# Optimization experiments

Hardware: AMD Instinct MI355X
Metric: run time of the kernel (lower is better)

The kernel has to match this reference:

```python
import jax, jax.numpy as jnp
import numpy as np

N = 100000   # nodes
E = 1600000  # edges
G = 1024     # graphs
V = 51       # attr_dims[0]+1 embedding rows (padding_idx=0)
EMB = 32
H = 2        # heads
D = 64       # hidden_dim (per-head out channels)
DC = H * D   # 128 = dim_conv
NEG_GAT = 0.2   # PyG GATConv default negative_slope
NEG_ACT = 0.05  # module's leaky_relu slope
LN_EPS = 1e-5


def setup_inputs() -> dict:
    key = jax.random.key(0)
    ks = jax.random.split(key, 20)
    def nrm(k, shape, scale=0.1):
        return jax.random.normal(k, shape, dtype=jnp.float32) * scale
    x = jax.random.randint(ks[0], (N, 1), 0, V)
    edge_index = jax.random.randint(ks[1], (2, E), 0, N)
    batch_idx = jnp.sort(jax.random.randint(ks[2], (N,), 0, G))
    return {
        'x': x, 'edge_index': edge_index, 'batch_idx': batch_idx,
        'emb': nrm(ks[3], (V, EMB)).at[0].set(0.0),  # padding_idx=0
        'ln_g': jnp.ones((EMB,), jnp.float32), 'ln_b': jnp.zeros((EMB,), jnp.float32),
        'W1': nrm(ks[4], (EMB, DC)), 'a_src1': nrm(ks[5], (H, D)), 'a_dst1': nrm(ks[6], (H, D)), 'b1': nrm(ks[7], (DC,)),
        'W2': nrm(ks[8], (DC, DC)), 'a_src2': nrm(ks[9], (H, D)), 'a_dst2': nrm(ks[10], (H, D)), 'b2': nrm(ks[11], (DC,)),
        'gw1': nrm(ks[12], (DC, D)), 'gb1': nrm(ks[13], (D,)),
        'gw2': nrm(ks[14], (D, 1)), 'gb2': nrm(ks[15], (1,)),
    }


def _gat_conv(xf, src, dst, W, a_src, a_dst, b):
    # xf: [N, in]; returns [N, H*D]. PyG GATConv, eval mode (attn dropout off).
    xw = (xf @ W).reshape(N, H, D)                           # [N,H,D]
    al_s = jnp.einsum('nhd,hd->nh', xw, a_src)
    al_d = jnp.einsum('nhd,hd->nh', xw, a_dst)
    e = jax.nn.leaky_relu(al_s[src] + al_d[dst], NEG_GAT)    # [E',H]
    m = jax.ops.segment_max(e, dst, num_segments=N)
    ex = jnp.exp(e - m[dst])
    s = jax.ops.segment_sum(ex, dst, num_segments=N)
    alpha = ex / s[dst]                                      # segment softmax over incoming edges
    msg = xw[src] * alpha[:, :, None]                        # [E',H,D]
    out = jax.ops.segment_sum(msg, dst, num_segments=N)      # [N,H,D]
    return out.reshape(N, DC) + b


def reference(x, edge_index, batch_idx, emb, ln_g, ln_b,
              W1, a_src1, a_dst1, b1, W2, a_src2, a_dst2, b2,
              gw1, gb1, gw2, gb2):
    # embedding + LayerNorm (dropout off in eval)
    xe = emb[x[:, 0]]                                        # [N,32]
    mu = jnp.mean(xe, axis=-1, keepdims=True)
    var = jnp.var(xe, axis=-1, keepdims=True)
    xe = (xe - mu) * jax.lax.rsqrt(var + LN_EPS) * ln_g + ln_b
    # add self loops (GATConv add_self_loops=True)
    ar = jnp.arange(N, dtype=edge_index.dtype)
    src = jnp.concatenate([edge_index[0], ar])
    dst = jnp.concatenate([edge_index[1], ar])
    h = jax.nn.leaky_relu(_gat_conv(xe, src, dst, W1, a_src1, a_dst1, b1), NEG_ACT)
    h = _gat_conv(h, src, dst, W2, a_src2, a_dst2, b2)       # [N,128]
    # attentional aggregation over graphs
    gate = jax.nn.leaky_relu(h @ gw1 + gb1, NEG_ACT) @ gw2 + gb2   # [N,1]
    gm = jax.ops.segment_max(gate, batch_idx, num_segments=G)
    ge = jnp.exp(gate - gm[batch_idx])
    gs = jax.ops.segment_sum(ge, batch_idx, num_segments=G)
    w = ge / gs[batch_idx]
    z = jax.ops.segment_sum(w * h, batch_idx, num_segments=G)      # [G,128]
    return h, z
```

## Files before the change

### kernel.cpp

```cpp
#include <hip/hip_runtime.h>
#include <hip/hip_bf16.h>
#include <stdint.h>

typedef unsigned short u16;
typedef unsigned int   u32;
typedef __attribute__((ext_vector_type(8))) short bf16x8;
typedef __attribute__((ext_vector_type(4))) float f32x4;

#define NEG_GAT 0.2f
#define NEG_ACT 0.05f
#define LN_EPS  1e-5f
#define NPARAM  15

__device__ __forceinline__ float bf2f(u32 bits16){
  union { u32 u; float f; } v; v.u = bits16 << 16; return v.f;
}
__device__ __forceinline__ u16 f2bf(float f){
  union { float f; u32 u; } v; v.f = f;
  u32 u = v.u;
  u32 r = (u + 0x7fffu + ((u >> 16) & 1u)) >> 16;
  return (u16)r;
}
__device__ __forceinline__ float lrelu(float x, float s){ return fmaxf(x, s * x); }

__device__ __forceinline__ int geti(const int* __restrict__ p, int i, int enc){
  return p[enc ? (2 * i) : i];
}


struct CvtParams {
  const void* src[NPARAM];
  float*      dst[NPARAM];
  int         n[NPARAM];
};

#define MAXB  2048

__global__ void k_detect(const u32* __restrict__ ln_g_raw, const int* __restrict__ ei_raw,
                         int* __restrict__ flags, int* __restrict__ bcnt)
{
  const int t = threadIdx.x;
  for (int i = t; i < MAXB; i += 256) bcnt[i] = 0;
  if (t == 0){
    flags[0] = (ln_g_raw[0] == 0x3F800000u) ? 0 : 1;
    int zeros = 0;
    for (int j = 0; j < 64; j++) if (ei_raw[2 * j + 1] == 0) zeros++;
    flags[1] = (zeros >= 60) ? 1 : 0;
    flags[2] = 0;
    flags[3] = 0;
  }
}

__global__ void k_convert(CvtParams P, const int* __restrict__ flag)
{
  const int pi  = blockIdx.y;
  const int idx = blockIdx.x * 256 + threadIdx.x;
  if (idx >= P.n[pi]) return;
  if (*flag == 0) P.dst[pi][idx] = ((const float*)P.src[pi])[idx];
  else            P.dst[pi][idx] = bf2f(((const u16*)P.src[pi])[idx]);
}


__global__ void k_checks(const int* __restrict__ batch, const int* __restrict__ x,
                         const int* __restrict__ iflag,
                         int n, int V, int* __restrict__ errflag)
{
  int i = blockIdx.x * 256 + threadIdx.x;
  const int enc = *iflag;
  if (i < n){
    int v = geti(x, i, enc);
    if ((unsigned)v >= (unsigned)V) atomicOr(errflag, 16);
    if (i < n - 1 && geti(batch, i, enc) > geti(batch, i + 1, enc)) atomicOr(errflag, 8);
  }
}

__global__ void k_check_edges(const int* __restrict__ ei, const int* __restrict__ iflag,
                              int E, int n, int* __restrict__ errflag)
{
  int e = blockIdx.x * 256 + threadIdx.x;
  if (e < E){
    int enc = *iflag;
    int s = geti(ei, e, enc);
    int d = geti(ei, E + e, enc);
    if ((unsigned)s >= (unsigned)n || (unsigned)d >= (unsigned)n) atomicOr(errflag, 32);
  }
}


__global__ void k_hist(const int* __restrict__ ei, const int* __restrict__ iflag,
                       int* __restrict__ counts, int E, int n)
{
  int e = blockIdx.x * 256 + threadIdx.x;
  if (e < E){
    int d = geti(ei, E + e, *iflag);
    d = min(max(d, 0), n - 1);
    atomicAdd(&counts[d], 1);
  }
}

__global__ void k_scanA(const int* __restrict__ counts, int* __restrict__ rowptr,
                        int* __restrict__ bsums, int n)
{
  __shared__ int sd[1024];
  int tid = threadIdx.x;
  int gid = blockIdx.x * 1024 + tid;
  int v = (gid < n) ? counts[gid] : 0;
  sd[tid] = v;
  __syncthreads();
  for (int off = 1; off < 1024; off <<= 1){
    int t = 0;
    if (tid >= off) t = sd[tid - off];
    __syncthreads();
    if (tid >= off) sd[tid] += t;
    __syncthreads();
  }
  if (gid < n) rowptr[gid] = sd[tid] - v;
  if (tid == 1023) bsums[blockIdx.x] = sd[1023];
}

__global__ void k_scanB(const int* __restrict__ bsums, int* __restrict__ boffs, int nb)
{
  __shared__ int sd[128];
  int tid = threadIdx.x;
  int v = (tid < nb) ? bsums[tid] : 0;
  sd[tid] = v;
  __syncthreads();
  for (int off = 1; off < 128; off <<= 1){
    int t = 0;
    if (tid >= off) t = sd[tid - off];
    __syncthreads();
    if (tid >= off) sd[tid] += t;
    __syncthreads();
  }
  if (tid < nb) boffs[tid] = sd[tid] - v;
}

__global__ void k_scanC(int* __restrict__ rowptr, const int* __restrict__ boffs,
                        int* __restrict__ cursor, int n, int Etot)
{
  int gid = blockIdx.x * 1024 + threadIdx.x;
  if (gid < n){
    int v = rowptr[gid] + boffs[blockIdx.x];
    rowptr[gid] = v;
    cursor[gid] = v;
  }
  if (gid == 0) rowptr[n] = Etot;
}

__global__ void k_scatter(const int* __restrict__ ei, const int* __restrict__ iflag,
                          int* __restrict__ cursor, int* __restrict__ csr, int E, int n)
{
  int e = blockIdx.x * 256 + threadIdx.x;
  if (e < E){
    int enc = *iflag;
    int s = geti(ei, e, enc);
    int d = geti(ei, E + e, enc);
    d = min(max(d, 0), n - 1);
    int pos = atomicAdd(&cursor[d], 1);
    csr[pos] = s;
  }
}

__global__ void k_check_rows(const int* __restrict__ rowptr, const int* __restrict__ cursor,
                             int n, int* __restrict__ errflag)
{
  int i = blockIdx.x * 256 + threadIdx.x;
  if (i < n){
    if (cursor[i] != rowptr[i + 1]) atomicOr(errflag, 1);
    if (i == 0 && rowptr[0] != 0)   atomicOr(errflag, 4);
  }
}

__global__ void k_check_csr(const int* __restrict__ csr, int E, int n, int* __restrict__ errflag)
{
  int e = blockIdx.x * 256 + threadIdx.x;
  if (e < E && (unsigned)csr[e] >= (unsigned)n) atomicOr(errflag, 2);
}


#define BSH   9
#define BSZ   512
#define BMSK  511
#define BINB  8192
#define BTH   512

__global__ void k_bhist(const int* __restrict__ ei, const int* __restrict__ iflag,
                        int* __restrict__ bcnt, int E, int N, int nbuck)
{
  __shared__ int h[MAXB];
  const int t = threadIdx.x;
  for (int i = t; i < nbuck; i += 256) h[i] = 0;
  __syncthreads();
  const int enc = *iflag;
  for (int e = blockIdx.x * 256 + t; e < E; e += gridDim.x * 256){
    int d = geti(ei, E + e, enc);
    d = min(max(d, 0), N - 1);
    atomicAdd(&h[d >> BSH], 1);
  }
  __syncthreads();
  for (int i = t; i < nbuck; i += 256){
    int c = h[i];
    if (c) atomicAdd(&bcnt[i], c);
  }
}

__global__ void k_bscan(const int* __restrict__ bcnt, int* __restrict__ boff,
                        int* __restrict__ gcur, int* __restrict__ rowptr,
                        int nbuck, int N, int E)
{
  __shared__ int sd[MAXB];
  const int lane = threadIdx.x;
  for (int i = lane; i < nbuck; i += 64) sd[i] = bcnt[i];
  __syncthreads();
  const int L = (nbuck + 63) >> 6;
  const int b0 = lane * L;
  int sum = 0;
  for (int j = 0; j < L; j++){ int idx = b0 + j; if (idx < nbuck) sum += sd[idx]; }
  int excl = sum;
  for (int off = 1; off < 64; off <<= 1){
    int x = __shfl_up(excl, off);
    if (lane >= off) excl += x;
  }
  excl -= sum;
  int run = excl;
  for (int j = 0; j < L; j++){
    int idx = b0 + j;
    if (idx < nbuck){ boff[idx] = run; gcur[idx] = run; run += sd[idx]; }
  }
  if (lane == 0){ boff[nbuck] = E; rowptr[N] = E; }
}

__global__ __launch_bounds__(BTH) void k_bbin(
    const int* __restrict__ ei, const int* __restrict__ iflag,
    int* __restrict__ gcur, u32* __restrict__ binned,
    int E, int N, int nbuck, int* __restrict__ errflag)
{
  __shared__ u32 stage[BINB];
  __shared__ u16 sbk[BINB];
  __shared__ int hist[MAXB];
  __shared__ int base[MAXB];
  __shared__ int gpos[MAXB];
  const int t   = threadIdx.x;
  const int e0  = blockIdx.x * BINB;
  const int cnt = min(BINB, E - e0);
  const int enc = *iflag;

  for (int i = t; i < nbuck; i += BTH) hist[i] = 0;
  __syncthreads();

  u32 pv[16]; int bk[16]; int rk[16];
  int bad = 0;
  #pragma unroll
  for (int k = 0; k < 16; k++){
    bk[k] = -1;
    int lo = k * BTH + t;
    if (lo < cnt){
      int e = e0 + lo;
      int s = geti(ei, e, enc);
      int d = geti(ei, E + e, enc);
      if ((unsigned)s >= (unsigned)N || (unsigned)d >= (unsigned)N) bad = 1;
      s = min(max(s, 0), N - 1);
      d = min(max(d, 0), N - 1);
      int b = d >> BSH;
      pv[k] = ((u32)s << BSH) | (u32)(d & BMSK);
      bk[k] = b;
      rk[k] = atomicAdd(&hist[b], 1);
    }
  }
  if (bad) atomicOr(errflag, 32);
  __syncthreads();

  if (t < 64){
    const int L = (nbuck + 63) >> 6;
    const int b0 = t * L;
    int sum = 0;
    for (int j = 0; j < L; j++){ int idx = b0 + j; if (idx < nbuck) sum += hist[idx]; }
    int excl = sum;
    for (int off = 1; off < 64; off <<= 1){
      int x = __shfl_up(excl, off);
      if (t >= off) excl += x;
    }
    excl -= sum;
    int run = excl;
    for (int j = 0; j < L; j++){
      int idx = b0 + j;
      if (idx < nbuck){ base[idx] = run; run += hist[idx]; }
    }
  }
  __syncthreads();

  for (int i = t; i < nbuck; i += BTH){
    int c = hist[i];
    gpos[i] = c ? atomicAdd(&gcur[i], c) : 0;
  }
  __syncthreads();

  #pragma unroll
  for (int k = 0; k < 16; k++){
    if (bk[k] >= 0){
      int slot = base[bk[k]] + rk[k];
      stage[slot] = pv[k];
      sbk[slot]   = (u16)bk[k];
    }
  }
  __syncthreads();

  for (int j = t; j < cnt; j += BTH){
    int b = sbk[j];
    binned[gpos[b] + (j - base[b])] = stage[j];
  }
}

__global__ __launch_bounds__(256) void k_bcsr(
    const u32* __restrict__ binned, const int* __restrict__ boff,
    int* __restrict__ rowptr, int* __restrict__ csr, int N, int nbuck)
{
  __shared__ int cnt[BSZ];
  __shared__ int rp[BSZ];
  __shared__ int cur[BSZ];
  const int b = blockIdx.x;
  const int t = threadIdx.x;
  const int lo = boff[b], hi = boff[b + 1];

  for (int i = t; i < BSZ; i += 256){ cnt[i] = 0; cur[i] = 0; }
  __syncthreads();

  for (int j = lo + t; j < hi; j += 256)
    atomicAdd(&cnt[binned[j] & BMSK], 1);
  __syncthreads();

  if (t < 64){
    const int b0 = t * 8;
    int sum = 0;
    #pragma unroll
    for (int j = 0; j < 8; j++) sum += cnt[b0 + j];
    int excl = sum;
    for (int off = 1; off < 64; off <<= 1){
      int x = __shfl_up(excl, off);
      if (t >= off) excl += x;
    }
    excl -= sum;
    int run = excl;
    #pragma unroll
    for (int j = 0; j < 8; j++){ rp[b0 + j] = run; run += cnt[b0 + j]; }
  }
  __syncthreads();

  const int node0 = b << BSH;
  for (int i = t; i < BSZ; i += 256){
    int node = node0 + i;
    if (node < N) rowptr[node] = lo + rp[i];
  }

  for (int j = lo + t; j < hi; j += 256){
    u32 pvv = binned[j];
    int dl  = pvv & BMSK;
    int pos = lo + rp[dl] + atomicAdd(&cur[dl], 1);
    csr[pos] = (int)(pvv >> BSH);
  }
}


__global__ void k_stamp_if(const int* __restrict__ errflag, float* __restrict__ out, int nel)
{
  int f = *errflag;
  if (f == 0) return;
  float s = 500.0f + 100.0f * (float)f;
  for (int i = blockIdx.x * 256 + threadIdx.x; i < nel; i += gridDim.x * 256) out[i] = s;
}

__global__ void k_stamp(float* __restrict__ out, int nel, float val)
{
  for (int i = blockIdx.x * 256 + threadIdx.x; i < nel; i += gridDim.x * 256) out[i] = val;
}


__global__ __launch_bounds__(128) void k_tables(
    const float* __restrict__ emb,
    const float* __restrict__ ln_g, const float* __restrict__ ln_b,
    const float* __restrict__ W1, const float* __restrict__ a_src,
    const float* __restrict__ a_dst,
    const float* __restrict__ W2, const float* __restrict__ gw1,
    int V,
    u16* __restrict__ xwv, float* __restrict__ alsv, float* __restrict__ aldv,
    u16* __restrict__ pb2, u16* __restrict__ pbg)
{
  const int bid = blockIdx.x;
  const int t   = threadIdx.x;

  if (bid >= V){
    if (t >= 64) return;
    int pw = bid - V;
    const float* W; int ncols, ntiles, blk; u16* pb;
    if (pw < 32){ W = W2; ncols = 128; ntiles = 8; blk = pw;      pb = pb2; }
    else        { W = gw1; ncols = 64;  ntiles = 4; blk = pw - 32; pb = pbg; }
    const int ktile = blk / ntiles;
    const int ntile = blk % ntiles;
    const int n  = ntile * 16 + (t & 15);
    const int k0 = ktile * 32 + (t >> 4) * 8;
    u16* dst = pb + ((size_t)blk * 64 + t) * 8;
    #pragma unroll
    for (int j = 0; j < 8; j++)
      dst[j] = f2bf(W[(k0 + j) * ncols + n]);
    return;
  }

  __shared__ float se[32];
  __shared__ float stats[2];
  __shared__ float sxw[128];
  const int v = bid;
  if (t < 32) se[t] = emb[v * 32 + t];
  __syncthreads();
  if (t == 0){
    float s1 = 0.f, s2 = 0.f;
    for (int k = 0; k < 32; k++){ s1 += se[k]; s2 += se[k] * se[k]; }
    float mu = s1 * (1.f / 32.f);
    float var = s2 * (1.f / 32.f) - mu * mu;
    stats[0] = mu; stats[1] = rsqrtf(var + LN_EPS);
  }
  __syncthreads();
  const float mu = stats[0], rs = stats[1];
  float o = 0.f;
  for (int k = 0; k < 32; k++){
    float xe = (se[k] - mu) * rs * ln_g[k] + ln_b[k];
    o += xe * W1[k * 128 + t];
  }
  sxw[t] = o;
  xwv[v * 128 + t] = f2bf(o);
  __syncthreads();
  if (t < 2){
    float ps = 0.f, pd = 0.f;
    for (int d = 0; d < 64; d++){
      float vv = sxw[t * 64 + d];
      ps += vv * a_src[t * 64 + d];
      pd += vv * a_dst[t * 64 + d];
    }
    alsv[2 * v + t] = ps;
    aldv[2 * v + t] = pd;
  }
}


__global__ __launch_bounds__(256, 4) void k_gatw1(
    const int* __restrict__ rowptr, const int* __restrict__ csr,
    const int* __restrict__ x, const int* __restrict__ iflag,
    const float* __restrict__ alsv, const float* __restrict__ aldv,
    const u16* __restrict__ xwv, const float* __restrict__ bias,
    int N, int V, u16* __restrict__ out)
{
  extern __shared__ char smem[];
  u16*    sxwv  = (u16*)smem;
  float2* sals  = (float2*)(smem + (size_t)V * 256);
  float2* sald  = sals + V;
  float4* sedge = (float4*)(smem + (size_t)V * 256 + (size_t)V * 16);

  const int tid = threadIdx.x;
  const int enc = *iflag;

  {
    const uint4* gx = (const uint4*)xwv;
    uint4* lx = (uint4*)sxwv;
    for (int idx = tid; idx < V * 16; idx += 256) lx[idx] = gx[idx];
    const float2* ga = (const float2*)alsv;
    const float2* gd = (const float2*)aldv;
    for (int idx = tid; idx < V; idx += 256){ sals[idx] = ga[idx]; sald[idx] = gd[idx]; }
  }
  __syncthreads();

  const int wave = tid >> 6;
  const int lane = tid & 63;
  const int sub  = lane >> 4;
  const int c16  = lane & 15;
  float4* mst = sedge + wave * 64;

  for (int i = blockIdx.x * 4 + wave; i < N; i += gridDim.x * 4){
    const int r0 = rowptr[i], deg = rowptr[i + 1] - r0, total = deg + 1;
    int vi = geti(x, i, enc); vi = min(max(vi, 0), V - 1);
    const float2 ad = sald[vi];

    float sum0 = 0.f, sum1 = 0.f;
    float acc[8];
    #pragma unroll
    for (int r = 0; r < 8; r++) acc[r] = 0.f;

    if (total <= 64){
      int vs = vi;
      float a0 = -3.0e38f, a1 = -3.0e38f;
      if (lane < total){
        int s = (lane < deg) ? csr[r0 + lane] : i;
        int v = geti(x, s, enc);
        vs = min(max(v, 0), V - 1);
        float2 as = sals[vs];
        a0 = lrelu(as.x + ad.x, NEG_GAT);
        a1 = lrelu(as.y + ad.y, NEG_GAT);
      }
      float m0 = a0, m1 = a1;
      #pragma unroll
      for (int off = 32; off; off >>= 1){
        m0 = fmaxf(m0, __shfl_xor(m0, off));
        m1 = fmaxf(m1, __shfl_xor(m1, off));
      }
      float ex0 = 0.f, ex1 = 0.f;
      if (lane < total){ ex0 = __expf(a0 - m0); ex1 = __expf(a1 - m1); }
      sum0 = ex0; sum1 = ex1;
      mst[lane] = make_float4(__int_as_float(vs), ex0, ex1, 0.f);
      int qmax = (total + 3) & ~3;
      for (int q = 0; q < qmax; q += 4){
        float4 md = mst[q + sub];
        int   vj = __float_as_int(md.x);
        float ej = (c16 < 8) ? md.y : md.z;
        uint4 w = *(const uint4*)(sxwv + vj * 128 + c16 * 8);
        acc[0] += ej * bf2f(w.x & 0xffffu); acc[1] += ej * bf2f(w.x >> 16);
        acc[2] += ej * bf2f(w.y & 0xffffu); acc[3] += ej * bf2f(w.y >> 16);
        acc[4] += ej * bf2f(w.z & 0xffffu); acc[5] += ej * bf2f(w.z >> 16);
        acc[6] += ej * bf2f(w.w & 0xffffu); acc[7] += ej * bf2f(w.w >> 16);
      }
    } else {
      float m0 = -3.0e38f, m1 = -3.0e38f;
      for (int k = lane; k < total; k += 64){
        int s = (k < deg) ? csr[r0 + k] : i;
        int v = geti(x, s, enc); v = min(max(v, 0), V - 1);
        float2 as = sals[v];
        m0 = fmaxf(m0, lrelu(as.x + ad.x, NEG_GAT));
        m1 = fmaxf(m1, lrelu(as.y + ad.y, NEG_GAT));
      }
      #pragma unroll
      for (int off = 32; off; off >>= 1){
        m0 = fmaxf(m0, __shfl_xor(m0, off));
        m1 = fmaxf(m1, __shfl_xor(m1, off));
      }
      for (int base = 0; base < total; base += 64){
        int k = base + lane;
        int vs = vi; float ex0 = 0.f, ex1 = 0.f;
        if (k < total){
          int s = (k < deg) ? csr[r0 + k] : i;
          int v = geti(x, s, enc); vs = min(max(v, 0), V - 1);
          float2 as = sals[vs];
          ex0 = __expf(lrelu(as.x + ad.x, NEG_GAT) - m0);
          ex1 = __expf(lrelu(as.y + ad.y, NEG_GAT) - m1);
        }
        sum0 += ex0; sum1 += ex1;
        mst[lane] = make_float4(__int_as_float(vs), ex0, ex1, 0.f);
        int cnt = min(64, total - base);
        int qmax = (cnt + 3) & ~3;
        for (int q = 0; q < qmax; q += 4){
          float4 md = mst[q + sub];
          int   vj = __float_as_int(md.x);
          float ej = (c16 < 8) ? md.y : md.z;
          uint4 w = *(const uint4*)(sxwv + vj * 128 + c16 * 8);
          acc[0] += ej * bf2f(w.x & 0xffffu); acc[1] += ej * bf2f(w.x >> 16);
          acc[2] += ej * bf2f(w.y & 0xffffu); acc[3] += ej * bf2f(w.y >> 16);
          acc[4] += ej * bf2f(w.z & 0xffffu); acc[5] += ej * bf2f(w.z >> 16);
          acc[6] += ej * bf2f(w.w & 0xffffu); acc[7] += ej * bf2f(w.w >> 16);
        }
      }
    }

    #pragma unroll
    for (int off = 32; off; off >>= 1){
      sum0 += __shfl_xor(sum0, off);
      sum1 += __shfl_xor(sum1, off);
    }
    #pragma unroll
    for (int r = 0; r < 8; r++){
      acc[r] += __shfl_xor(acc[r], 16);
      acc[r] += __shfl_xor(acc[r], 32);
    }

    if (sub == 0){
      float inv = 1.f / ((c16 < 8) ? sum0 : sum1);
      const float4* bp = (const float4*)(bias + c16 * 8);
      float4 b0 = bp[0], b1 = bp[1];
      float o[8];
      o[0] = lrelu(acc[0] * inv + b0.x, NEG_ACT); o[1] = lrelu(acc[1] * inv + b0.y, NEG_ACT);
      o[2] = lrelu(acc[2] * inv + b0.z, NEG_ACT); o[3] = lrelu(acc[3] * inv + b0.w, NEG_ACT);
      o[4] = lrelu(acc[4] * inv + b1.x, NEG_ACT); o[5] = lrelu(acc[5] * inv + b1.y, NEG_ACT);
      o[6] = lrelu(acc[6] * inv + b1.z, NEG_ACT); o[7] = lrelu(acc[7] * inv + b1.w, NEG_ACT);
      uint4 pk;
      pk.x = (u32)f2bf(o[0]) | ((u32)f2bf(o[1]) << 16);
      pk.y = (u32)f2bf(o[2]) | ((u32)f2bf(o[3]) << 16);
      pk.z = (u32)f2bf(o[4]) | ((u32)f2bf(o[5]) << 16);
      pk.w = (u32)f2bf(o[6]) | ((u32)f2bf(o[7]) << 16);
      *(uint4*)(out + (size_t)i * 128 + c16 * 8) = pk;
    }
  }
}

__global__ __launch_bounds__(64, 8) void k_gatw1g(
    const int* __restrict__ rowptr, const int* __restrict__ csr,
    const int* __restrict__ x, const int* __restrict__ iflag,
    const float* __restrict__ alsv, const float* __restrict__ aldv,
    const u16* __restrict__ xwv, const float* __restrict__ bias,
    int V, u16* __restrict__ out)
{
  const int i    = blockIdx.x;
  const int lane = threadIdx.x;
  const int sub  = lane >> 4;
  const int c16  = lane & 15;
  const int enc  = *iflag;
  const int r0 = rowptr[i], deg = rowptr[i + 1] - r0, total = deg + 1;
  int vi = geti(x, i, enc); vi = min(max(vi, 0), V - 1);
  const float ad0 = aldv[2 * vi], ad1 = aldv[2 * vi + 1];

  float sum0 = 0.f, sum1 = 0.f;
  float acc[8];
  #pragma unroll
  for (int r = 0; r < 8; r++) acc[r] = 0.f;

  float m0 = -3.0e38f, m1 = -3.0e38f;
  for (int k = lane; k < total; k += 64){
    int s = (k < deg) ? csr[r0 + k] : i;
    int v = geti(x, s, enc); v = min(max(v, 0), V - 1);
    float2 as = *(const float2*)(alsv + 2 * v);
    m0 = fmaxf(m0, lrelu(as.x + ad0, NEG_GAT));
    m1 = fmaxf(m1, lrelu(as.y + ad1, NEG_GAT));
  }
  #pragma unroll
  for (int off = 32; off; off >>= 1){
    m0 = fmaxf(m0, __shfl_xor(m0, off));
    m1 = fmaxf(m1, __shfl_xor(m1, off));
  }
  for (int base = 0; base < total; base += 64){
    int k = base + lane;
    int vs = vi; float ex0 = 0.f, ex1 = 0.f;
    if (k < total){
      int s = (k < deg) ? csr[r0 + k] : i;
      int v = geti(x, s, enc); vs = min(max(v, 0), V - 1);
      float2 as = *(const float2*)(alsv + 2 * vs);
      ex0 = __expf(lrelu(as.x + ad0, NEG_GAT) - m0);
      ex1 = __expf(lrelu(as.y + ad1, NEG_GAT) - m1);
    }
    sum0 += ex0; sum1 += ex1;
    int cnt = min(64, total - base);
    int qmax = (cnt + 3) & ~3;
    for (int q = 0; q < qmax; q += 4){
      int   j  = q + sub;
      int   vj = __shfl(vs, j);
      float e0 = __shfl(ex0, j);
      float e1 = __shfl(ex1, j);
      float ej = (c16 < 8) ? e0 : e1;
      uint4 w = *(const uint4*)(xwv + (size_t)vj * 128 + c16 * 8);
      acc[0] += ej * bf2f(w.x & 0xffffu); acc[1] += ej * bf2f(w.x >> 16);
      acc[2] += ej * bf2f(w.y & 0xffffu); acc[3] += ej * bf2f(w.y >> 16);
      acc[4] += ej * bf2f(w.z & 0xffffu); acc[5] += ej * bf2f(w.z >> 16);
      acc[6] += ej * bf2f(w.w & 0xffffu); acc[7] += ej * bf2f(w.w >> 16);
    }
  }

  #pragma unroll
  for (int off = 32; off; off >>= 1){
    sum0 += __shfl_xor(sum0, off);
    sum1 += __shfl_xor(sum1, off);
  }
  #pragma unroll
  for (int r = 0; r < 8; r++){
    acc[r] += __shfl_xor(acc[r], 16);
    acc[r] += __shfl_xor(acc[r], 32);
  }

  if (sub == 0){
    float inv = 1.f / ((c16 < 8) ? sum0 : sum1);
    const float4* bp = (const float4*)(bias + c16 * 8);
    float4 b0 = bp[0], b1 = bp[1];
    float o[8];
    o[0] = lrelu(acc[0] * inv + b0.x, NEG_ACT); o[1] = lrelu(acc[1] * inv + b0.y, NEG_ACT);
    o[2] = lrelu(acc[2] * inv + b0.z, NEG_ACT); o[3] = lrelu(acc[3] * inv + b0.w, NEG_ACT);
    o[4] = lrelu(acc[4] * inv + b1.x, NEG_ACT); o[5] = lrelu(acc[5] * inv + b1.y, NEG_ACT);
    o[6] = lrelu(acc[6] * inv + b1.z, NEG_ACT); o[7] = lrelu(acc[7] * inv + b1.w, NEG_ACT);
    uint4 pk;
    pk.x = (u32)f2bf(o[0]) | ((u32)f2bf(o[1]) << 16);
    pk.y = (u32)f2bf(o[2]) | ((u32)f2bf(o[3]) << 16);
    pk.z = (u32)f2bf(o[4]) | ((u32)f2bf(o[5]) << 16);
    pk.w = (u32)f2bf(o[6]) | ((u32)f2bf(o[7]) << 16);
    *(uint4*)(out + (size_t)i * 128 + c16 * 8) = pk;
  }
}


__global__ __launch_bounds__(64, 8) void k_gatw2(
    const int* __restrict__ rowptr, const int* __restrict__ csr,
    const float* __restrict__ al_s, const float* __restrict__ al_d,
    const u16* __restrict__ xw, const float* __restrict__ bias,
    int apply_act, float* __restrict__ out)
{
  const int i    = blockIdx.x;
  const int lane = threadIdx.x;
  const int sub  = lane >> 4;
  const int c16  = lane & 15;
  const int r0 = rowptr[i], deg = rowptr[i + 1] - r0, total = deg + 1;
  const float2 ad = *(const float2*)(al_d + 2 * i);

  float sum0 = 0.f, sum1 = 0.f;
  float acc[8];
  #pragma unroll
  for (int r = 0; r < 8; r++) acc[r] = 0.f;

  if (total <= 64){
    int s = i;
    float a0 = -3.0e38f, a1 = -3.0e38f;
    if (lane < total){
      s = (lane < deg) ? csr[r0 + lane] : i;
      float2 as = *(const float2*)(al_s + 2 * s);
      a0 = lrelu(as.x + ad.x, NEG_GAT);
      a1 = lrelu(as.y + ad.y, NEG_GAT);
    }
    float m0 = a0, m1 = a1;
    #pragma unroll
    for (int off = 32; off; off >>= 1){
      m0 = fmaxf(m0, __shfl_xor(m0, off));
      m1 = fmaxf(m1, __shfl_xor(m1, off));
    }
    float ex0 = 0.f, ex1 = 0.f;
    if (lane < total){ ex0 = __expf(a0 - m0); ex1 = __expf(a1 - m1); }
    sum0 = ex0; sum1 = ex1;
    int qmax = (total + 3) & ~3;
    for (int q = 0; q < qmax; q += 4){
      int   j  = q + sub;
      int   sj = __shfl(s, j);
      float e0 = __shfl(ex0, j);
      float e1 = __shfl(ex1, j);
      float ej = (c16 < 8) ? e0 : e1;
      uint4 w = *(const uint4*)(xw + (size_t)sj * 128 + c16 * 8);
      acc[0] += ej * bf2f(w.x & 0xffffu); acc[1] += ej * bf2f(w.x >> 16);
      acc[2] += ej * bf2f(w.y & 0xffffu); acc[3] += ej * bf2f(w.y >> 16);
      acc[4] += ej * bf2f(w.z & 0xffffu); acc[5] += ej * bf2f(w.z >> 16);
      acc[6] += ej * bf2f(w.w & 0xffffu); acc[7] += ej * bf2f(w.w >> 16);
    }
  } else {
    float m0 = -3.0e38f, m1 = -3.0e38f;
    for (int k = lane; k < total; k += 64){
      int s = (k < deg) ? csr[r0 + k] : i;
      float2 as = *(const float2*)(al_s + 2 * s);
      m0 = fmaxf(m0, lrelu(as.x + ad.x, NEG_GAT));
      m1 = fmaxf(m1, lrelu(as.y + ad.y, NEG_GAT));
    }
    #pragma unroll
    for (int off = 32; off; off >>= 1){
      m0 = fmaxf(m0, __shfl_xor(m0, off));
      m1 = fmaxf(m1, __shfl_xor(m1, off));
    }
    for (int base = 0; base < total; base += 64){
      int k = base + lane;
      int s = i; float ex0 = 0.f, ex1 = 0.f;
      if (k < total){
        s = (k < deg) ? csr[r0 + k] : i;
        float2 as = *(const float2*)(al_s + 2 * s);
        ex0 = __expf(lrelu(as.x + ad.x, NEG_GAT) - m0);
        ex1 = __expf(lrelu(as.y + ad.y, NEG_GAT) - m1);
      }
      sum0 += ex0; sum1 += ex1;
      int cnt = min(64, total - base);
      int qmax = (cnt + 3) & ~3;
      for (int q = 0; q < qmax; q += 4){
        int   j  = q + sub;
        int   sj = __shfl(s, j);
        float e0 = __shfl(ex0, j);
        float e1 = __shfl(ex1, j);
        float ej = (c16 < 8) ? e0 : e1;
        uint4 w = *(const uint4*)(xw + (size_t)sj * 128 + c16 * 8);
        acc[0] += ej * bf2f(w.x & 0xffffu); acc[1] += ej * bf2f(w.x >> 16);
        acc[2] += ej * bf2f(w.y & 0xffffu); acc[3] += ej * bf2f(w.y >> 16);
        acc[4] += ej * bf2f(w.z & 0xffffu); acc[5] += ej * bf2f(w.z >> 16);
        acc[6] += ej * bf2f(w.w & 0xffffu); acc[7] += ej * bf2f(w.w >> 16);
      }
    }
  }

  #pragma unroll
  for (int off = 32; off; off >>= 1){
    sum0 += __shfl_xor(sum0, off);
    sum1 += __shfl_xor(sum1, off);
  }
  #pragma unroll
  for (int r = 0; r < 8; r++){
    acc[r] += __shfl_xor(acc[r], 16);
    acc[r] += __shfl_xor(acc[r], 32);
  }

  if (sub == 0){
    float inv = 1.f / ((c16 < 8) ? sum0 : sum1);
    const float4* bp = (const float4*)(bias + c16 * 8);
    float4 b0 = bp[0], b1 = bp[1];
    float4 o0, o1;
    o0.x = acc[0] * inv + b0.x; o0.y = acc[1] * inv + b0.y;
    o0.z = acc[2] * inv + b0.z; o0.w = acc[3] * inv + b0.w;
    o1.x = acc[4] * inv + b1.x; o1.y = acc[5] * inv + b1.y;
    o1.z = acc[6] * inv + b1.z; o1.w = acc[7] * inv + b1.w;
    if (apply_act){
      o0.x = lrelu(o0.x, NEG_ACT); o0.y = lrelu(o0.y, NEG_ACT);
      o0.z = lrelu(o0.z, NEG_ACT); o0.w = lrelu(o0.w, NEG_ACT);
      o1.x = lrelu(o1.x, NEG_ACT); o1.y = lrelu(o1.y, NEG_ACT);
      o1.z = lrelu(o1.z, NEG_ACT); o1.w = lrelu(o1.w, NEG_ACT);
    }
    float* op = out + (size_t)i * 128 + c16 * 8;
    *(float4*)op       = o0;
    *(float4*)(op + 4) = o1;
  }
}


__global__ __launch_bounds__(256, 2) void k_node2m(
    const u16* __restrict__ h1b, const u16* __restrict__ pb2,
    const float* __restrict__ a_src, const float* __restrict__ a_dst,
    int N, u16* __restrict__ xw, float* __restrict__ al_s, float* __restrict__ al_d)
{
  const int wave = threadIdx.x >> 6;
  const int lane = threadIdx.x & 63;
  const int rowbase = blockIdx.x * 64 + wave * 16;
  const int m    = lane & 15;
  const int quad = lane >> 4;

  int arow = rowbase + m; if (arow >= N) arow = N - 1;
  const u16* aptr = h1b + (size_t)arow * 128 + quad * 8;

  f32x4 acc[8];
  #pragma unroll
  for (int nt = 0; nt < 8; nt++) acc[nt] = (f32x4){0.f, 0.f, 0.f, 0.f};

  #pragma unroll
  for (int kt = 0; kt < 4; kt++){
    bf16x8 af = *(const bf16x8*)(aptr + kt * 32);
    const u16* bbase = pb2 + (((size_t)kt * 8) * 64 + lane) * 8;
    #pragma unroll
    for (int nt = 0; nt < 8; nt++){
      bf16x8 bf = *(const bf16x8*)(bbase + (size_t)nt * 64 * 8);
      acc[nt] = __builtin_amdgcn_mfma_f32_16x16x32_bf16(af, bf, acc[nt], 0, 0, 0);
    }
  }

  float asv[8], adv[8];
  #pragma unroll
  for (int nt = 0; nt < 8; nt++){
    asv[nt] = a_src[nt * 16 + m];
    adv[nt] = a_dst[nt * 16 + m];
  }
  #pragma unroll
  for (int r = 0; r < 4; r++){
    int row = rowbase + quad * 4 + r;
    bool ok = row < N;
    float s0 = 0.f, s1 = 0.f, d0 = 0.f, d1 = 0.f;
    #pragma unroll
    for (int nt = 0; nt < 8; nt++){
      float v = acc[nt][r];
      if (ok) xw[(size_t)row * 128 + nt * 16 + m] = f2bf(v);
      if (nt < 4){ s0 += v * asv[nt]; d0 += v * adv[nt]; }
      else       { s1 += v * asv[nt]; d1 += v * adv[nt]; }
    }
    #pragma unroll
    for (int off = 1; off < 16; off <<= 1){
      s0 += __shfl_xor(s0, off); s1 += __shfl_xor(s1, off);
      d0 += __shfl_xor(d0, off); d1 += __shfl_xor(d1, off);
    }
    if (ok && m == 0){
      al_s[2 * row] = s0; al_s[2 * row + 1] = s1;
      al_d[2 * row] = d0; al_d[2 * row + 1] = d1;
    }
  }
}


__global__ __launch_bounds__(256, 2) void k_gatem(
    const float* __restrict__ h, const u16* __restrict__ pbg,
    const float* __restrict__ gb1, const float* __restrict__ gw2,
    const float* __restrict__ gb2, int N, float* __restrict__ gate)
{
  const int wave = threadIdx.x >> 6;
  const int lane = threadIdx.x & 63;
  const int rowbase = blockIdx.x * 64 + wave * 16;
  const int m    = lane & 15;
  const int quad = lane >> 4;

  int arow = rowbase + m; if (arow >= N) arow = N - 1;
  const float* aptr = h + (size_t)arow * 128 + quad * 8;

  f32x4 acc[4];
  #pragma unroll
  for (int nt = 0; nt < 4; nt++) acc[nt] = (f32x4){0.f, 0.f, 0.f, 0.f};

  #pragma unroll
  for (int kt = 0; kt < 4; kt++){
    float4 a0 = *(const float4*)(aptr + kt * 32);
    float4 a1 = *(const float4*)(aptr + kt * 32 + 4);
    bf16x8 af;
    af[0] = (short)f2bf(a0.x); af[1] = (short)f2bf(a0.y);
    af[2] = (short)f2bf(a0.z); af[3] = (short)f2bf(a0.w);
    af[4] = (short)f2bf(a1.x); af[5] = (short)f2bf(a1.y);
    af[6] = (short)f2bf(a1.z); af[7] = (short)f2bf(a1.w);
    const u16* bbase = pbg + (((size_t)kt * 4) * 64 + lane) * 8;
    #pragma unroll
    for (int nt = 0; nt < 4; nt++){
      bf16x8 bf = *(const bf16x8*)(bbase + (size_t)nt * 64 * 8);
      acc[nt] = __builtin_amdgcn_mfma_f32_16x16x32_bf16(af, bf, acc[nt], 0, 0, 0);
    }
  }

  float gbv[4], g2v[4];
  #pragma unroll
  for (int nt = 0; nt < 4; nt++){
    gbv[nt] = gb1[nt * 16 + m];
    g2v[nt] = gw2[nt * 16 + m];
  }
  const float g2b = gb2[0];
  #pragma unroll
  for (int r = 0; r < 4; r++){
    int row = rowbase + quad * 4 + r;
    float q = 0.f;
    #pragma unroll
    for (int nt = 0; nt < 4; nt++)
      q += lrelu(acc[nt][r] + gbv[nt], NEG_ACT) * g2v[nt];
    #pragma unroll
    for (int off = 1; off < 16; off <<= 1) q += __shfl_xor(q, off);
    if (row < N && m == 0) gate[row] = q + g2b;
  }
}


__global__ __launch_bounds__(512) void k_graphsw(
    const int* __restrict__ batch, const int* __restrict__ iflag,
    const float* __restrict__ gate,
    const float* __restrict__ h, float* __restrict__ zout, int N)
{
  __shared__ int   range[2];
  __shared__ float red[16];
  __shared__ float sz[3][128];
  const int g = blockIdx.x, t = threadIdx.x;
  const int wave = t >> 6, lane = t & 63;
  if (t == 0){
    const int enc = *iflag;
    int lo = 0, hi = N;
    while (lo < hi){ int mid = (lo + hi) >> 1; if (geti(batch, mid, enc) < g) lo = mid + 1; else hi = mid; }
    range[0] = lo;
    hi = N;
    while (lo < hi){ int mid = (lo + hi) >> 1; if (geti(batch, mid, enc) < g + 1) lo = mid + 1; else hi = mid; }
    range[1] = lo;
  }
  __syncthreads();
  const int st = range[0], en = range[1];

  float m = -3.0e38f;
  for (int k = st + t; k < en; k += 512) m = fmaxf(m, gate[k]);
  #pragma unroll
  for (int off = 32; off; off >>= 1) m = fmaxf(m, __shfl_xor(m, off));
  if (lane == 0) red[wave] = m;
  __syncthreads();
  m = red[0];
  #pragma unroll
  for (int w = 1; w < 8; w++) m = fmaxf(m, red[w]);

  float s = 0.f;
  for (int k = st + t; k < en; k += 512) s += __expf(gate[k] - m);
  #pragma unroll
  for (int off = 32; off; off >>= 1) s += __shfl_xor(s, off);
  if (lane == 0) red[8 + wave] = s;
  __syncthreads();
  s = red[8];
  #pragma unroll
  for (int w = 9; w < 16; w++) s += red[w];

  const float inv = 1.f / s;
  const int quarter = t >> 7, t2 = t & 127;
  float z = 0.f;
  for (int k = st + quarter; k < en; k += 4){
    float wk = __expf(gate[k] - m) * inv;
    z += wk * h[(size_t)k * 128 + t2];
  }
  if (quarter) sz[quarter - 1][t2] = z;
  __syncthreads();
  if (quarter == 0) zout[(size_t)g * 128 + t2] = z + sz[0][t2] + sz[1][t2] + sz[2][t2];
}


extern "C" void kernel_launch(void* const* d_in, const int* in_sizes, int n_in,
                              void* d_out, int out_size, void* d_ws, size_t ws_size,
                              hipStream_t stream)
{
  const int* x      = (const int*)d_in[0];
  const int* ei     = (const int*)d_in[1];
  const int* batch  = (const int*)d_in[2];

  const int N = in_sizes[0];
  const int E = in_sizes[1] / 2;
  const int V = in_sizes[3] / 32;
  const int G = out_size / 128 - N;

  char* p = (char*)d_ws;
  auto alloc = [&](size_t bytes) -> char* {
    char* r = p; p += (bytes + 255) & ~(size_t)255; return r;
  };
  int*   multi  = (int*)  alloc((size_t)N * 4);
  int*   rowptr = (int*)  alloc((size_t)(N + 1) * 4);
  int*   csr    = (int*)  alloc((size_t)E * 4);
  int*   bsums  = (int*)  alloc(4096);
  int*   boffs  = (int*)  alloc(4096);
  int*   flags  = (int*)  alloc(256);
  int*   fflag  = flags;
  int*   iflag  = flags + 1;
  int*   errflg = flags + 2;
  float* al_s   = (float*)alloc((size_t)N * 2 * 4);
  float* al_d   = (float*)alloc((size_t)N * 2 * 4);
  u16*   xw     = (u16*)  alloc((size_t)N * 128 * 2);
  u16*   h1b    = (u16*)  alloc((size_t)N * 128 * 2);
  u16*   xwv    = (u16*)  alloc((size_t)V * 128 * 2);
  float* alsv   = (float*)alloc((size_t)V * 2 * 4);
  float* aldv   = (float*)alloc((size_t)V * 2 * 4);
  u16*   pb2    = (u16*)  alloc((size_t)128 * 128 * 2);
  u16*   pbg    = (u16*)  alloc((size_t)128 * 64 * 2);

  const int nbuck = (N + BSZ - 1) >> BSH;
  int*   bcnt   = (int*)  alloc((size_t)(MAXB) * 4);
  int*   boff   = (int*)  alloc((size_t)(MAXB + 1) * 4);
  int*   gcur   = (int*)  alloc((size_t)(MAXB) * 4);
  u32*   binned = (u32*)  alloc((size_t)E * 4);

  CvtParams cp;
  float* fpar[NPARAM];
  int maxn = 0;
  for (int pi = 0; pi < NPARAM; pi++){
    int n = in_sizes[3 + pi];
    fpar[pi] = (float*)alloc((size_t)n * 4);
    cp.src[pi] = d_in[3 + pi];
    cp.dst[pi] = fpar[pi];
    cp.n[pi]   = n;
    if (n > maxn) maxn = n;
  }
  const size_t needed = (size_t)(p - (char*)d_ws);

  const float* emb    = fpar[0];
  const float* ln_g   = fpar[1];
  const float* ln_b   = fpar[2];
  const float* W1     = fpar[3];
  const float* a_src1 = fpar[4];
  const float* a_dst1 = fpar[5];
  const float* b1     = fpar[6];
  const float* W2     = fpar[7];
  const float* a_src2 = fpar[8];
  const float* a_dst2 = fpar[9];
  const float* b2     = fpar[10];
  const float* gw1    = fpar[11];
  const float* gb1    = fpar[12];
  const float* gw2    = fpar[13];
  const float* gb2    = fpar[14];
  (void)n_in;

  if (ws_size < needed){
    k_stamp<<<512, 256, 0, stream>>>((float*)d_out, out_size, 9999.0f);
    return;
  }

  int*   counts = multi;
  int*   cursor = multi;
  float* gate   = (float*)multi;
  float* hbuf   = (float*)d_out;
  float* zbuf   = (float*)d_out + (size_t)N * 128;

  k_detect<<<1, 256, 0, stream>>>((const u32*)d_in[4], ei, flags, bcnt);
  dim3 cgrid((maxn + 255) / 256, NPARAM);
  k_convert<<<cgrid, 256, 0, stream>>>(cp, fflag);

  int eb = (E + 255) / 256;
  int nb = (N + 1023) / 1024;
  int nb256 = (N + 255) / 256;

  k_checks<<<nb256, 256, 0, stream>>>(batch, x, iflag, N, V, errflg);

  if (nbuck <= MAXB){
    k_bhist<<<256, 256, 0, stream>>>(ei, iflag, bcnt, E, N, nbuck);
    k_bscan<<<1, 64, 0, stream>>>(bcnt, boff, gcur, rowptr, nbuck, N, E);
    k_bbin<<<(E + BINB - 1) / BINB, BTH, 0, stream>>>(ei, iflag, gcur, binned, E, N, nbuck, errflg);
    k_bcsr<<<nbuck, 256, 0, stream>>>(binned, boff, rowptr, csr, N, nbuck);
  } else {
    k_check_edges<<<eb, 256, 0, stream>>>(ei, iflag, E, N, errflg);
    hipMemsetAsync(counts, 0, (size_t)N * 4, stream);
    hipMemsetAsync(csr, 0xFF, (size_t)E * 4, stream);
    k_hist<<<eb, 256, 0, stream>>>(ei, iflag, counts, E, N);
    k_scanA<<<nb, 1024, 0, stream>>>(counts, rowptr, bsums, N);
    k_scanB<<<1, 128, 0, stream>>>(bsums, boffs, nb);
    k_scanC<<<nb, 1024, 0, stream>>>(rowptr, boffs, cursor, N, E);
    k_scatter<<<eb, 256, 0, stream>>>(ei, iflag, cursor, csr, E, N);
    k_check_rows<<<nb256, 256, 0, stream>>>(rowptr, cursor, N, errflg);
    k_check_csr<<<eb, 256, 0, stream>>>(csr, E, N, errflg);
  }

  k_tables<<<V + 48, 128, 0, stream>>>(emb, ln_g, ln_b, W1, a_src1, a_dst1,
                                       W2, gw1, V, xwv, alsv, aldv, pb2, pbg);

  const int gwb = min(2048, (N + 3) / 4);
  const size_t smem1 = (size_t)V * 272 + 4096;
  if (smem1 <= 64 * 1024){
    k_gatw1<<<gwb, 256, smem1, stream>>>(rowptr, csr, x, iflag, alsv, aldv, xwv, b1, N, V, h1b);
  } else {
    k_gatw1g<<<N, 64, 0, stream>>>(rowptr, csr, x, iflag, alsv, aldv, xwv, b1, V, h1b);
  }

  const int gblk = (N + 63) / 64;
  k_node2m<<<gblk, 256, 0, stream>>>(h1b, pb2, a_src2, a_dst2, N, xw, al_s, al_d);

  k_gatw2<<<N, 64, 0, stream>>>(rowptr, csr, al_s, al_d, xw, b2, 0, hbuf);

  k_gatem<<<gblk, 256, 0, stream>>>(hbuf, pbg, gb1, gw2, gb2, N, gate);
  k_graphsw<<<G, 512, 0, stream>>>(batch, iflag, gate, hbuf, zbuf, N);

  k_stamp_if<<<512, 256, 0, stream>>>(errflg, (float*)d_out, out_size);
}
```

Measured before the change: 352.6 us.

## Precompute per-vocab attention exp table for layer-1 GAT in shared memory

```diff
diff --git a/kernel.cpp b/kernel.cpp
--- a/kernel.cpp
+++ b/kernel.cpp
@@ -382,7 +382,8 @@
     const float* __restrict__ a_dst,
     const float* __restrict__ W2, const float* __restrict__ gw1,
     int V,
-    u16* __restrict__ xwv, float* __restrict__ alsv, float* __restrict__ aldv,
+    u16* __restrict__ xwv, float* __restrict__ xwvf,
+    float* __restrict__ alsv, float* __restrict__ aldv,
     u16* __restrict__ pb2, u16* __restrict__ pbg)
 {
   const int bid = blockIdx.x;
@@ -426,7 +427,8 @@
     o += xe * W1[k * 128 + t];
   }
   sxw[t] = o;
-  xwv[v * 128 + t] = f2bf(o);
+  xwv[v * 128 + t]  = f2bf(o);
+  xwvf[v * 128 + t] = o;
   __syncthreads();
   if (t < 2){
     float ps = 0.f, pd = 0.f;
@@ -441,29 +443,45 @@
 }
 
 
-__global__ __launch_bounds__(256, 4) void k_gatw1(
+__global__ __launch_bounds__(256, 3) void k_gatw1(
     const int* __restrict__ rowptr, const int* __restrict__ csr,
     const int* __restrict__ x, const int* __restrict__ iflag,
     const float* __restrict__ alsv, const float* __restrict__ aldv,
-    const u16* __restrict__ xwv, const float* __restrict__ bias,
+    const float* __restrict__ xwvf, const float* __restrict__ bias,
     int N, int V, u16* __restrict__ out)
 {
   extern __shared__ char smem[];
-  u16*    sxwv  = (u16*)smem;
-  float2* sals  = (float2*)(smem + (size_t)V * 256);
-  float2* sald  = sals + V;
-  float4* sedge = (float4*)(smem + (size_t)V * 256 + (size_t)V * 16);
+  float4* sedge = (float4*)smem;
+  float*  srow  = (float*)(smem + 4096);
+  float*  ET    = srow + (size_t)V * 128;
 
   const int tid = threadIdx.x;
   const int enc = *iflag;
 
   {
-    const uint4* gx = (const uint4*)xwv;
-    uint4* lx = (uint4*)sxwv;
-    for (int idx = tid; idx < V * 16; idx += 256) lx[idx] = gx[idx];
-    const float2* ga = (const float2*)alsv;
-    const float2* gd = (const float2*)aldv;
-    for (int idx = tid; idx < V; idx += 256){ sals[idx] = ga[idx]; sald[idx] = gd[idx]; }
+    const float4* gx = (const float4*)xwvf;
+    float4* lx = (float4*)srow;
+    for (int idx = tid; idx < V * 32; idx += 256) lx[idx] = gx[idx];
+  }
+  {
+    const int tot = V * V;
+    for (int idx = tid; idx < tot; idx += 256){
+      int vi = idx / V, v = idx - vi * V;
+      ET[idx * 2]     = lrelu(alsv[2 * v]     + aldv[2 * vi],     NEG_GAT);
+      ET[idx * 2 + 1] = lrelu(alsv[2 * v + 1] + aldv[2 * vi + 1], NEG_GAT);
+    }
+  }
+  __syncthreads();
+  {
+    for (int r = tid; r < V * 2; r += 256){
+      int vi = r >> 1, h = r & 1;
+      float m = -3.0e38f;
+      for (int v = 0; v < V; v++) m = fmaxf(m, ET[(vi * V + v) * 2 + h]);
+      for (int v = 0; v < V; v++){
+        int idx = (vi * V + v) * 2 + h;
+        ET[idx] = __expf(ET[idx] - m);
+      }
+    }
   }
   __syncthreads();
 
@@ -476,83 +494,37 @@
   for (int i = blockIdx.x * 4 + wave; i < N; i += gridDim.x * 4){
     const int r0 = rowptr[i], deg = rowptr[i + 1] - r0, total = deg + 1;
     int vi = geti(x, i, enc); vi = min(max(vi, 0), V - 1);
-    const float2 ad = sald[vi];
+    const float* ETrow = ET + (size_t)vi * V * 2;
 
     float sum0 = 0.f, sum1 = 0.f;
     float acc[8];
     #pragma unroll
     for (int r = 0; r < 8; r++) acc[r] = 0.f;
 
-    if (total <= 64){
-      int vs = vi;
-      float a0 = -3.0e38f, a1 = -3.0e38f;
-      if (lane < total){
-        int s = (lane < deg) ? csr[r0 + lane] : i;
+    for (int base = 0; base < total; base += 64){
+      int k = base + lane;
+      int vs = vi; float w0 = 0.f, w1 = 0.f;
+      if (k < total){
+        int s = (k < deg) ? csr[r0 + k] : i;
         int v = geti(x, s, enc);
         vs = min(max(v, 0), V - 1);
-        float2 as = sals[vs];
-        a0 = lrelu(as.x + ad.x, NEG_GAT);
-        a1 = lrelu(as.y + ad.y, NEG_GAT);
+        w0 = ETrow[vs * 2];
+        w1 = ETrow[vs * 2 + 1];
       }
-      float m0 = a0, m1 = a1;
-      #pragma unroll
-      for (int off = 32; off; off >>= 1){
-        m0 = fmaxf(m0, __shfl_xor(m0, off));
-        m1 = fmaxf(m1, __shfl_xor(m1, off));
-      }
-      float ex0 = 0.f, ex1 = 0.f;
-      if (lane < total){ ex0 = __expf(a0 - m0); ex1 = __expf(a1 - m1); }
-      sum0 = ex0; sum1 = ex1;
-      mst[lane] = make_float4(__int_as_float(vs), ex0, ex1, 0.f);
-      int qmax = (total + 3) & ~3;
+      sum0 += w0; sum1 += w1;
+      mst[lane] = make_float4(__int_as_float(vs), w0, w1, 0.f);
+      int cnt = min(64, total - base);
+      int qmax = (cnt + 3) & ~3;
       for (int q = 0; q < qmax; q += 4){
         float4 md = mst[q + sub];
         int   vj = __float_as_int(md.x);
         float ej = (c16 < 8) ? md.y : md.z;
-        uint4 w = *(const uint4*)(sxwv + vj * 128 + c16 * 8);
-        acc[0] += ej * bf2f(w.x & 0xffffu); acc[1] += ej * bf2f(w.x >> 16);
-        acc[2] += ej * bf2f(w.y & 0xffffu); acc[3] += ej * bf2f(w.y >> 16);
-        acc[4] += ej * bf2f(w.z & 0xffffu); acc[5] += ej * bf2f(w.z >> 16);
-        acc[6] += ej * bf2f(w.w & 0xffffu); acc[7] += ej * bf2f(w.w >> 16);
-      }
-    } else {
-      float m0 = -3.0e38f, m1 = -3.0e38f;
-      for (int k = lane; k < total; k += 64){
-        int s = (k < deg) ? csr[r0 + k] : i;
-        int v = geti(x, s, enc); v = min(max(v, 0), V - 1);
-        float2 as = sals[v];
-        m0 = fmaxf(m0, lrelu(as.x + ad.x, NEG_GAT));
-        m1 = fmaxf(m1, lrelu(as.y + ad.y, NEG_GAT));
-      }
-      #pragma unroll
-      for (int off = 32; off; off >>= 1){
-        m0 = fmaxf(m0, __shfl_xor(m0, off));
-        m1 = fmaxf(m1, __shfl_xor(m1, off));
-      }
-      for (int base = 0; base < total; base += 64){
-        int k = base + lane;
-        int vs = vi; float ex0 = 0.f, ex1 = 0.f;
-        if (k < total){
-          int s = (k < deg) ? csr[r0 + k] : i;
-          int v = geti(x, s, enc); vs = min(max(v, 0), V - 1);
-          float2 as = sals[vs];
-          ex0 = __expf(lrelu(as.x + ad.x, NEG_GAT) - m0);
-          ex1 = __expf(lrelu(as.y + ad.y, NEG_GAT) - m1);
-        }
-        sum0 += ex0; sum1 += ex1;
-        mst[lane] = make_float4(__int_as_float(vs), ex0, ex1, 0.f);
-        int cnt = min(64, total - base);
-        int qmax = (cnt + 3) & ~3;
-        for (int q = 0; q < qmax; q += 4){
-          float4 md = mst[q + sub];
-          int   vj = __float_as_int(md.x);
-          float ej = (c16 < 8) ? md.y : md.z;
-          uint4 w = *(const uint4*)(sxwv + vj * 128 + c16 * 8);
-          acc[0] += ej * bf2f(w.x & 0xffffu); acc[1] += ej * bf2f(w.x >> 16);
-          acc[2] += ej * bf2f(w.y & 0xffffu); acc[3] += ej * bf2f(w.y >> 16);
-          acc[4] += ej * bf2f(w.z & 0xffffu); acc[5] += ej * bf2f(w.z >> 16);
-          acc[6] += ej * bf2f(w.w & 0xffffu); acc[7] += ej * bf2f(w.w >> 16);
-        }
+        const float4* rp = (const float4*)(srow + (size_t)vj * 128 + c16 * 8);
+        float4 wa = rp[0], wb = rp[1];
+        acc[0] += ej * wa.x; acc[1] += ej * wa.y;
+        acc[2] += ej * wa.z; acc[3] += ej * wa.w;
+        acc[4] += ej * wb.x; acc[5] += ej * wb.y;
+        acc[6] += ej * wb.z; acc[7] += ej * wb.w;
       }
     }
 
@@ -1001,6 +973,7 @@
   u16*   xw     = (u16*)  alloc((size_t)N * 128 * 2);
   u16*   h1b    = (u16*)  alloc((size_t)N * 128 * 2);
   u16*   xwv    = (u16*)  alloc((size_t)V * 128 * 2);
+  float* xwvf   = (float*)alloc((size_t)V * 128 * 4);
   float* alsv   = (float*)alloc((size_t)V * 2 * 4);
   float* aldv   = (float*)alloc((size_t)V * 2 * 4);
   u16*   pb2    = (u16*)  alloc((size_t)128 * 128 * 2);
@@ -1082,12 +1055,12 @@
   }
 
   k_tables<<<V + 48, 128, 0, stream>>>(emb, ln_g, ln_b, W1, a_src1, a_dst1,
-                                       W2, gw1, V, xwv, alsv, aldv, pb2, pbg);
-
-  const int gwb = min(2048, (N + 3) / 4);
-  const size_t smem1 = (size_t)V * 272 + 4096;
-  if (smem1 <= 64 * 1024){
-    k_gatw1<<<gwb, 256, smem1, stream>>>(rowptr, csr, x, iflag, alsv, aldv, xwv, b1, N, V, h1b);
+                                       W2, gw1, V, xwv, xwvf, alsv, aldv, pb2, pbg);
+
+  const size_t smem1 = 4096 + (size_t)V * 512 + (size_t)V * V * 8;
+  if (V <= 64 && smem1 <= 64 * 1024){
+    const int gwb = min(768, (N + 3) / 4);
+    k_gatw1<<<gwb, 256, smem1, stream>>>(rowptr, csr, x, iflag, alsv, aldv, xwvf, b1, N, V, h1b);
   } else {
     k_gatw1g<<<N, 64, 0, stream>>>(rowptr, csr, x, iflag, alsv, aldv, xwv, b1, V, h1b);
   }
```

Result: slower. 366.2 us (+3.9%).
